# Optimization experiments

Hardware: AMD Instinct MI355X
Metric: run time of the kernel (lower is better)

Reference implementation:

```python
import jax, jax.numpy as jnp
import numpy as np

N_EMBD = 1024
N_HEAD = 16
HEAD_DIM = N_EMBD // N_HEAD


def setup_inputs() -> dict:
    key = jax.random.key(0)
    kx, kqkv, kw, kb = jax.random.split(key, 4)
    B, T = 4, 2048
    x = jax.random.normal(kx, (B, T, N_EMBD), dtype=jnp.float32)
    # nn.Linear weights stored [out, in]; apply as x @ W.T
    w_qkv = jax.random.normal(kqkv, (3 * N_EMBD, N_EMBD), dtype=jnp.float32) * (N_EMBD ** -0.5)
    w_out = jax.random.normal(kw, (N_EMBD, N_EMBD), dtype=jnp.float32) * (N_EMBD ** -0.5)
    b_out = jax.random.normal(kb, (N_EMBD,), dtype=jnp.float32) * 0.01
    return {"x": x, "w_qkv": w_qkv, "w_out": w_out, "b_out": b_out}


def reference(x, w_qkv, w_out, b_out):
    B, T, C = x.shape
    H, D = N_HEAD, HEAD_DIM
    qkv = jnp.einsum('btc,fc->btf', x, w_qkv)  # [B,T,3C]
    q, k, v = jnp.split(qkv, 3, axis=-1)
    q = q.reshape(B, T, H, D).transpose(0, 2, 1, 3)  # [B,H,T,D]
    k = k.reshape(B, T, H, D).transpose(0, 2, 1, 3)
    v = v.reshape(B, T, H, D).transpose(0, 2, 1, 3)
    att = jnp.einsum('bhqd,bhkd->bhqk', q, k) * (D ** -0.5)  # [B,H,T,T]
    causal = jnp.tril(jnp.ones((T, T), dtype=bool))
    att = jnp.where(causal[None, None], att, jnp.float32(-jnp.inf))
    att = jax.nn.softmax(att, axis=-1)
    out = jnp.einsum('bhqk,bhkd->bhqd', att, v)  # [B,H,T,D]
    out = out.transpose(0, 2, 1, 3).reshape(B, T, C)
    return jnp.einsum('btc,oc->bto', out, w_out) + b_out
```

## Files before the change

### kernel.cpp

```cpp
#include <hip/hip_runtime.h>
#include <stdint.h>

#define SEQ 2048
#define C3 3072
#define C1 1024

typedef __bf16 bf16x8 __attribute__((ext_vector_type(8)));
typedef short short8 __attribute__((ext_vector_type(8)));
typedef float f32x4 __attribute__((ext_vector_type(4)));
typedef float f32x16 __attribute__((ext_vector_type(16)));
typedef const __attribute__((address_space(1))) void gv_t;
typedef __attribute__((address_space(3))) void lv_t;

#if __has_builtin(__builtin_amdgcn_exp2f)
#define EXP2(x) __builtin_amdgcn_exp2f(x)
#else
#define EXP2(x) exp2f(x)
#endif

static __device__ __forceinline__ unsigned short f2bf(float f) {
  union { float ff; unsigned u; } x; x.ff = f;
  unsigned u = x.u + 0x7FFFu + ((x.u >> 16) & 1u);
  return (unsigned short)(u >> 16);
}
static __device__ __forceinline__ unsigned rne2(float lo, float hi) {
  return (unsigned)f2bf(lo) | ((unsigned)f2bf(hi) << 16);
}
static __device__ __forceinline__ unsigned pk2(float lo, float hi) {
  union { float f; unsigned u; } a, b; a.f = lo; b.f = hi;
  return __builtin_amdgcn_perm(b.u, a.u, 0x07060302);
}

__global__ void k_cvt3(const float* __restrict__ ia, const float* __restrict__ ib,
                       const float* __restrict__ ic, unsigned short* __restrict__ oa,
                       unsigned short* __restrict__ ob, unsigned short* __restrict__ oc) {
  int blk = blockIdx.x;
  const float* in; unsigned short* out; int base;
  if (blk < 8192)      { in = ia; out = oa; base = blk; }
  else if (blk < 11264){ in = ib; out = ob; base = blk - 8192; }
  else                 { in = ic; out = oc; base = blk - 11264; }
  int i = base * 256 + threadIdx.x;
  f32x4 v = ((const f32x4*)in)[i];
  ushort4 o;
  o.x = f2bf(v[0]); o.y = f2bf(v[1]); o.z = f2bf(v[2]); o.w = f2bf(v[3]);
  ((ushort4*)out)[i] = o;
}

template<int MODE>
__global__ __launch_bounds__(256, 3) void k_gemm(
    const unsigned short* __restrict__ A, const unsigned short* __restrict__ B,
    void* __restrict__ Cout, const float* __restrict__ bias,
    unsigned short* __restrict__ vTout, int M, int N, int K)
{
  __shared__ unsigned short As[128 * 64];
  __shared__ unsigned short Bs[128 * 64];
  const int tid = threadIdx.x;
  const int w = tid >> 6, l = tid & 63;
  const int lane15 = l & 15, quad = l >> 4;
  const int m0 = blockIdx.y * 128, n0 = blockIdx.x * 128;
  const int wm = (w >> 1) * 64, wn = (w & 1) * 64;

  f32x4 acc[4][4];
#pragma unroll
  for (int i = 0; i < 4; i++)
#pragma unroll
    for (int j = 0; j < 4; j++) acc[i][j] = (f32x4){0.f, 0.f, 0.f, 0.f};

  const int srow = l >> 3;
  const int g_off = ((l & 7) ^ (srow & 7)) * 8;
  const unsigned short* Ab = A + (size_t)(m0 + w * 32 + srow) * K + g_off;
  const unsigned short* Bb = B + (size_t)(n0 + w * 32 + srow) * K + g_off;
  const int rsl = lane15 & 7;

  for (int k0 = 0; k0 < K; k0 += 64) {
    __syncthreads();
#pragma unroll
    for (int i = 0; i < 4; i++) {
      int rb = w * 32 + i * 8;
      __builtin_amdgcn_global_load_lds((gv_t*)(Ab + (size_t)(i * 8) * K + k0),
                                       (lv_t*)&As[rb * 64], 16, 0, 0);
      __builtin_amdgcn_global_load_lds((gv_t*)(Bb + (size_t)(i * 8) * K + k0),
                                       (lv_t*)&Bs[rb * 64], 16, 0, 0);
    }
    __syncthreads();
#pragma unroll
    for (int s = 0; s < 2; s++) {
      bf16x8 af[4], bfr[4];
      const int slot = ((s * 4 + quad) ^ rsl) * 8;
#pragma unroll
      for (int t = 0; t < 4; t++) {
        af[t]  = *(const bf16x8*)&As[(wm + t * 16 + lane15) * 64 + slot];
        bfr[t] = *(const bf16x8*)&Bs[(wn + t * 16 + lane15) * 64 + slot];
      }
#pragma unroll
      for (int i = 0; i < 4; i++)
#pragma unroll
        for (int j = 0; j < 4; j++)
          acc[i][j] = __builtin_amdgcn_mfma_f32_16x16x32_bf16(af[i], bfr[j], acc[i][j], 0, 0, 0);
    }
  }

  if (MODE == 0) {
    if (n0 >= 2048) {
#pragma unroll
      for (int i = 0; i < 4; i++) {
        int rowb = m0 + wm + i * 16 + quad * 4;
        int bb = rowb >> 11, t = rowb & 2047;
#pragma unroll
        for (int j = 0; j < 4; j++) {
          int hd = n0 + wn + j * 16 + lane15 - 2048;
          unsigned short* vp = vTout +
              ((size_t)((bb << 4) + (hd >> 6)) * 64 + (hd & 63)) * SEQ + t;
          *(uint2*)vp = make_uint2(rne2(acc[i][j][0], acc[i][j][1]),
                                   rne2(acc[i][j][2], acc[i][j][3]));
        }
      }
    } else {
      unsigned short* Cp = (unsigned short*)Cout;
      const float s = (n0 < 1024) ? 0.18033688f : 1.0f;
#pragma unroll
      for (int i = 0; i < 4; i++) {
        int rowb = m0 + wm + i * 16 + quad * 4;
#pragma unroll
        for (int j = 0; j < 4; j++) {
          int col = n0 + wn + j * 16 + lane15;
#pragma unroll
          for (int r = 0; r < 4; r++)
            Cp[(size_t)(rowb + r) * N + col] = f2bf(acc[i][j][r] * s);
        }
      }
    }
  } else {
    float* Cp = (float*)Cout;
#pragma unroll
    for (int i = 0; i < 4; i++) {
      int rowb = m0 + wm + i * 16 + quad * 4;
#pragma unroll
      for (int j = 0; j < 4; j++) {
        int col = n0 + wn + j * 16 + lane15;
        float bv = bias[col];
#pragma unroll
        for (int r = 0; r < 4; r++)
          Cp[(size_t)(rowb + r) * N + col] = acc[i][j][r] + bv;
      }
    }
  }
}

__global__ __launch_bounds__(256, 4) void k_attn(
    const unsigned short* __restrict__ qkv, const unsigned short* __restrict__ vT,
    unsigned short* __restrict__ att)
{
  __shared__ unsigned short buf[16384];
  const int tid = threadIdx.x;
  const int w = tid >> 6, l = tid & 63;
  const int l31 = l & 31, hl = l >> 5;
  const int bh = blockIdx.x, b = bh >> 4, h = bh & 15;
  const int qt = (int)(gridDim.y - 1 - blockIdx.y);
  const int q0 = qt << 7;
  const int nkt = qt + 1;
  const size_t tokb = (size_t)b * SEQ;
  const int qmy = q0 + w * 32 + l31;

  bf16x8 qf[4];
  {
    const unsigned short* qp = qkv + (tokb + q0 + w * 32 + l31) * C3 + h * 64 + hl * 8;
#pragma unroll
    for (int ks = 0; ks < 4; ks++) qf[ks] = *(const bf16x8*)(qp + ks * 16);
  }

  f32x16 O[2];
#pragma unroll
  for (int i = 0; i < 16; i++) { O[0][i] = 0.f; O[1][i] = 0.f; }
  float lrun = 0.f;

  const int krow_l = l >> 3, kslot = l & 7;
  const int vrow_l = l >> 4, vslot = l & 15;
  unsigned short* Kb = &buf[0];
  unsigned short* Vb = &buf[8192];

  for (int kt = 0; kt < nkt; kt++) {
    const int k0 = kt << 7;
    __syncthreads();
#pragma unroll
    for (int i = 0; i < 4; i++) {
      int rb = (w * 4 + i) * 8;
      int row = rb + krow_l;
      int ck = kslot ^ (row & 7);
      const unsigned short* g = qkv + (tokb + k0 + row) * C3 + C1 + h * 64 + ck * 8;
      __builtin_amdgcn_global_load_lds((gv_t*)g, (lv_t*)&Kb[rb * 64], 16, 0, 0);
    }
#pragma unroll
    for (int i = 0; i < 4; i++) {
      int rb = (w * 4 + i) * 4;
      int row = rb + vrow_l;
      int ck = vslot ^ (row & 15);
      const unsigned short* g = vT + ((size_t)bh * 64 + row) * SEQ + k0 + ck * 8;
      __builtin_amdgcn_global_load_lds((gv_t*)g, (lv_t*)&Vb[rb * 128], 16, 0, 0);
    }
    __syncthreads();

    const bool diag = (kt == nkt - 1);

#pragma unroll
    for (int ht = 0; ht < 2; ht++) {
      if (diag && (ht * 2 > w)) continue;
      const bool two = !diag || (ht * 2 + 1 <= w);

#pragma unroll
      for (int lm = 0; lm < 2; lm++) {
        if (lm == 1 && !two) continue;
        const int mt = ht * 2 + lm;

        f32x16 stL;
#pragma unroll
        for (int i = 0; i < 16; i++) stL[i] = 0.f;
        {
          int row = mt * 32 + l31;
          const unsigned short* kr = &Kb[row * 64];
#pragma unroll
          for (int ks = 0; ks < 4; ks++) {
            bf16x8 a = *(const bf16x8*)&kr[((((ks << 1) | hl)) ^ (row & 7)) * 8];
            stL = __builtin_amdgcn_mfma_f32_32x32x16_bf16(a, qf[ks], stL, 0, 0, 0);
          }
        }

        if (diag && mt == w) {
#pragma unroll
          for (int r = 0; r < 16; r++) {
            int key = k0 + w * 32 + (r & 3) + ((r >> 2) << 3) + (hl << 2);
            if (key > qmy) stL[r] = -1e30f;
          }
        }

        float ps0 = 0.f, ps1 = 0.f, ps2 = 0.f, ps3 = 0.f;
        unsigned pk[8];
#pragma unroll
        for (int r = 0; r < 16; r += 4) {
          float p0 = EXP2(stL[r]     - 16.f);
          float p1 = EXP2(stL[r + 1] - 16.f);
          float p2 = EXP2(stL[r + 2] - 16.f);
          float p3 = EXP2(stL[r + 3] - 16.f);
          ps0 += p0; ps1 += p1; ps2 += p2; ps3 += p3;
          pk[(r >> 1)]     = pk2(p0, p1);
          pk[(r >> 1) + 1] = pk2(p2, p3);
        }
        lrun += (ps0 + ps1) + (ps2 + ps3);

#pragma unroll
        for (int e = 0; e < 2; e++) {
          unsigned pA0 = pk[4 * e], pA1 = pk[4 * e + 1];
          unsigned pB0 = pk[4 * e + 2], pB1 = pk[4 * e + 3];
          unsigned w0 = hl ? pA0 : pB0, w1 = hl ? pA1 : pB1;
          unsigned r0 = (unsigned)__shfl_xor((int)w0, 32, 64);
          unsigned r1 = (unsigned)__shfl_xor((int)w1, 32, 64);
          unsigned s0 = hl ? pB0 : pA0, s1 = hl ? pB1 : pA1;
          union { unsigned u[4]; bf16x8 v; } Bf;
          Bf.u[0] = hl ? r0 : s0; Bf.u[1] = hl ? r1 : s1;
          Bf.u[2] = hl ? s0 : r0; Bf.u[3] = hl ? s1 : r1;
          int kk = ht * 4 + lm * 2 + e;
#pragma unroll
          for (int dt = 0; dt < 2; dt++) {
            int row = dt * 32 + l31;
            bf16x8 a = *(const bf16x8*)&Vb[row * 128 + (((2 * kk + hl)) ^ (row & 15)) * 8];
            O[dt] = __builtin_amdgcn_mfma_f32_32x32x16_bf16(a, Bf.v, O[dt], 0, 0, 0);
          }
        }
      }
    }
  }

  lrun += __shfl_xor(lrun, 32, 64);

  __syncthreads();
  float linv = __builtin_amdgcn_rcpf(lrun);
  unsigned* epi32 = (unsigned*)&buf[0];
  const int base = w * 2304 + l31 * 72;
#pragma unroll
  for (int dt = 0; dt < 2; dt++)
#pragma unroll
    for (int c = 0; c < 4; c++) {
      int d0 = dt * 32 + c * 8 + hl * 4;
      epi32[(base + d0) >> 1]     = rne2(O[dt][4 * c] * linv, O[dt][4 * c + 1] * linv);
      epi32[(base + d0 + 2) >> 1] = rne2(O[dt][4 * c + 2] * linv, O[dt][4 * c + 3] * linv);
    }
  __builtin_amdgcn_s_waitcnt(0);
  {
    int q = l >> 1, hf = l & 1;
    const unsigned short* ep = &buf[w * 2304 + q * 72 + hf * 32];
    unsigned short* og = att + (tokb + q0 + w * 32 + q) * C1 + h * 64 + hf * 32;
#pragma unroll
    for (int c2 = 0; c2 < 4; c2++)
      *(bf16x8*)(og + c2 * 8) = *(const bf16x8*)&ep[c2 * 8];
  }
}

extern "C" void kernel_launch(void* const* d_in, const int* in_sizes, int n_in,
                              void* d_out, int out_size, void* d_ws, size_t ws_size,
                              hipStream_t stream) {
  const float* x     = (const float*)d_in[0];
  const float* w_qkv = (const float*)d_in[1];
  const float* w_out = (const float*)d_in[2];
  const float* b_out = (const float*)d_in[3];
  float* out = (float*)d_out;

  unsigned short* xb  = (unsigned short*)d_ws;
  unsigned short* wqb = xb  + (size_t)8192 * 1024;
  unsigned short* wob = wqb + (size_t)3072 * 1024;
  unsigned short* qkv = wob + (size_t)1024 * 1024;
  unsigned short* att = qkv + (size_t)8192 * 3072;
  unsigned short* vT  = att + (size_t)8192 * 1024;

  k_cvt3<<<12288, 256, 0, stream>>>(x, w_qkv, w_out, xb, wqb, wob);
  k_gemm<0><<<dim3(24, 64), 256, 0, stream>>>(xb, wqb, (void*)qkv, nullptr, vT, 8192, 3072, 1024);
  k_attn<<<dim3(64, 16), 256, 0, stream>>>(qkv, vT, att);
  k_gemm<1><<<dim3(8, 64), 256, 0, stream>>>(att, wob, (void*)out, b_out, nullptr, 8192, 1024, 1024);
}
```

Baseline: 230.3 us.

## Pair causal query tiles per block and double-buffer K/V staging

```diff
diff --git a/kernel.cpp b/kernel.cpp
--- a/kernel.cpp
+++ b/kernel.cpp
@@ -147,135 +147,119 @@
   }
 }
 
-__global__ __launch_bounds__(256, 4) void k_attn(
-    const unsigned short* __restrict__ qkv, const unsigned short* __restrict__ vT,
-    unsigned short* __restrict__ att)
-{
-  __shared__ unsigned short buf[16384];
-  const int tid = threadIdx.x;
-  const int w = tid >> 6, l = tid & 63;
-  const int l31 = l & 31, hl = l >> 5;
-  const int bh = blockIdx.x, b = bh >> 4, h = bh & 15;
-  const int qt = (int)(gridDim.y - 1 - blockIdx.y);
-  const int q0 = qt << 7;
-  const int nkt = qt + 1;
-  const size_t tokb = (size_t)b * SEQ;
-  const int qmy = q0 + w * 32 + l31;
-
-  bf16x8 qf[4];
-  {
-    const unsigned short* qp = qkv + (tokb + q0 + w * 32 + l31) * C3 + h * 64 + hl * 8;
-#pragma unroll
-    for (int ks = 0; ks < 4; ks++) qf[ks] = *(const bf16x8*)(qp + ks * 16);
-  }
-
-  f32x16 O[2];
-#pragma unroll
-  for (int i = 0; i < 16; i++) { O[0][i] = 0.f; O[1][i] = 0.f; }
-  float lrun = 0.f;
-
-  const int krow_l = l >> 3, kslot = l & 7;
-  const int vrow_l = l >> 4, vslot = l & 15;
-  unsigned short* Kb = &buf[0];
-  unsigned short* Vb = &buf[8192];
-
-  for (int kt = 0; kt < nkt; kt++) {
-    const int k0 = kt << 7;
-    __syncthreads();
-#pragma unroll
-    for (int i = 0; i < 4; i++) {
-      int rb = (w * 4 + i) * 8;
-      int row = rb + krow_l;
-      int ck = kslot ^ (row & 7);
-      const unsigned short* g = qkv + (tokb + k0 + row) * C3 + C1 + h * 64 + ck * 8;
-      __builtin_amdgcn_global_load_lds((gv_t*)g, (lv_t*)&Kb[rb * 64], 16, 0, 0);
-    }
-#pragma unroll
-    for (int i = 0; i < 4; i++) {
-      int rb = (w * 4 + i) * 4;
-      int row = rb + vrow_l;
-      int ck = vslot ^ (row & 15);
-      const unsigned short* g = vT + ((size_t)bh * 64 + row) * SEQ + k0 + ck * 8;
-      __builtin_amdgcn_global_load_lds((gv_t*)g, (lv_t*)&Vb[rb * 128], 16, 0, 0);
-    }
-    __syncthreads();
-
-    const bool diag = (kt == nkt - 1);
-
-#pragma unroll
-    for (int ht = 0; ht < 2; ht++) {
-      if (diag && (ht * 2 > w)) continue;
-      const bool two = !diag || (ht * 2 + 1 <= w);
-
-#pragma unroll
-      for (int lm = 0; lm < 2; lm++) {
-        if (lm == 1 && !two) continue;
-        const int mt = ht * 2 + lm;
-
-        f32x16 stL;
-#pragma unroll
-        for (int i = 0; i < 16; i++) stL[i] = 0.f;
-        {
-          int row = mt * 32 + l31;
-          const unsigned short* kr = &Kb[row * 64];
-#pragma unroll
-          for (int ks = 0; ks < 4; ks++) {
-            bf16x8 a = *(const bf16x8*)&kr[((((ks << 1) | hl)) ^ (row & 7)) * 8];
-            stL = __builtin_amdgcn_mfma_f32_32x32x16_bf16(a, qf[ks], stL, 0, 0, 0);
-          }
-        }
-
-        if (diag && mt == w) {
-#pragma unroll
-          for (int r = 0; r < 16; r++) {
-            int key = k0 + w * 32 + (r & 3) + ((r >> 2) << 3) + (hl << 2);
-            if (key > qmy) stL[r] = -1e30f;
-          }
-        }
-
-        float ps0 = 0.f, ps1 = 0.f, ps2 = 0.f, ps3 = 0.f;
-        unsigned pk[8];
-#pragma unroll
-        for (int r = 0; r < 16; r += 4) {
-          float p0 = EXP2(stL[r]     - 16.f);
-          float p1 = EXP2(stL[r + 1] - 16.f);
-          float p2 = EXP2(stL[r + 2] - 16.f);
-          float p3 = EXP2(stL[r + 3] - 16.f);
-          ps0 += p0; ps1 += p1; ps2 += p2; ps3 += p3;
-          pk[(r >> 1)]     = pk2(p0, p1);
-          pk[(r >> 1) + 1] = pk2(p2, p3);
-        }
-        lrun += (ps0 + ps1) + (ps2 + ps3);
-
-#pragma unroll
-        for (int e = 0; e < 2; e++) {
-          unsigned pA0 = pk[4 * e], pA1 = pk[4 * e + 1];
-          unsigned pB0 = pk[4 * e + 2], pB1 = pk[4 * e + 3];
-          unsigned w0 = hl ? pA0 : pB0, w1 = hl ? pA1 : pB1;
-          unsigned r0 = (unsigned)__shfl_xor((int)w0, 32, 64);
-          unsigned r1 = (unsigned)__shfl_xor((int)w1, 32, 64);
-          unsigned s0 = hl ? pB0 : pA0, s1 = hl ? pB1 : pA1;
-          union { unsigned u[4]; bf16x8 v; } Bf;
-          Bf.u[0] = hl ? r0 : s0; Bf.u[1] = hl ? r1 : s1;
-          Bf.u[2] = hl ? s0 : r0; Bf.u[3] = hl ? s1 : r1;
-          int kk = ht * 4 + lm * 2 + e;
-#pragma unroll
-          for (int dt = 0; dt < 2; dt++) {
-            int row = dt * 32 + l31;
-            bf16x8 a = *(const bf16x8*)&Vb[row * 128 + (((2 * kk + hl)) ^ (row & 15)) * 8];
-            O[dt] = __builtin_amdgcn_mfma_f32_32x32x16_bf16(a, Bf.v, O[dt], 0, 0, 0);
-          }
-        }
-      }
-    }
-  }
-
+
+static __device__ __forceinline__ void stage_kv(
+    unsigned short* bufp, const unsigned short* __restrict__ qkv,
+    const unsigned short* __restrict__ vT, size_t tokb, int bh, int h,
+    int k0, int w, int krow_l, int kslot, int vrow_l, int vslot)
+{
+  unsigned short* Kb = bufp;
+  unsigned short* Vb = bufp + 8192;
+#pragma unroll
+  for (int i = 0; i < 4; i++) {
+    int rb = (w * 4 + i) * 8;
+    int row = rb + krow_l;
+    int ck = kslot ^ (row & 7);
+    const unsigned short* g = qkv + (tokb + k0 + row) * C3 + C1 + h * 64 + ck * 8;
+    __builtin_amdgcn_global_load_lds((gv_t*)g, (lv_t*)&Kb[rb * 64], 16, 0, 0);
+  }
+#pragma unroll
+  for (int i = 0; i < 4; i++) {
+    int rb = (w * 4 + i) * 4;
+    int row = rb + vrow_l;
+    int ck = vslot ^ (row & 15);
+    const unsigned short* g = vT + ((size_t)bh * 64 + row) * SEQ + k0 + ck * 8;
+    __builtin_amdgcn_global_load_lds((gv_t*)g, (lv_t*)&Vb[rb * 128], 16, 0, 0);
+  }
+}
+
+static __device__ __forceinline__ void attn_tile(
+    f32x16* O, float& lrun, const bf16x8* qf,
+    const unsigned short* Kb, const unsigned short* Vb,
+    bool diag, int k0, int qmy, int w, int l31, int hl)
+{
+#pragma unroll
+  for (int ht = 0; ht < 2; ht++) {
+    if (diag && (ht * 2 > w)) continue;
+    const bool two = !diag || (ht * 2 + 1 <= w);
+
+#pragma unroll
+    for (int lm = 0; lm < 2; lm++) {
+      if (lm == 1 && !two) continue;
+      const int mt = ht * 2 + lm;
+
+      f32x16 stL;
+#pragma unroll
+      for (int i = 0; i < 16; i++) stL[i] = 0.f;
+      {
+        int row = mt * 32 + l31;
+        const unsigned short* kr = &Kb[row * 64];
+        __builtin_amdgcn_s_setprio(1);
+#pragma unroll
+        for (int ks = 0; ks < 4; ks++) {
+          bf16x8 a = *(const bf16x8*)&kr[((((ks << 1) | hl)) ^ (row & 7)) * 8];
+          stL = __builtin_amdgcn_mfma_f32_32x32x16_bf16(a, qf[ks], stL, 0, 0, 0);
+        }
+        __builtin_amdgcn_s_setprio(0);
+      }
+
+      if (diag && mt == w) {
+#pragma unroll
+        for (int r = 0; r < 16; r++) {
+          int key = k0 + w * 32 + (r & 3) + ((r >> 2) << 3) + (hl << 2);
+          if (key > qmy) stL[r] = -1e30f;
+        }
+      }
+
+      float ps0 = 0.f, ps1 = 0.f, ps2 = 0.f, ps3 = 0.f;
+      unsigned pk[8];
+#pragma unroll
+      for (int r = 0; r < 16; r += 4) {
+        float p0 = EXP2(stL[r]     - 16.f);
+        float p1 = EXP2(stL[r + 1] - 16.f);
+        float p2 = EXP2(stL[r + 2] - 16.f);
+        float p3 = EXP2(stL[r + 3] - 16.f);
+        ps0 += p0; ps1 += p1; ps2 += p2; ps3 += p3;
+        pk[(r >> 1)]     = pk2(p0, p1);
+        pk[(r >> 1) + 1] = pk2(p2, p3);
+      }
+      lrun += (ps0 + ps1) + (ps2 + ps3);
+
+#pragma unroll
+      for (int e = 0; e < 2; e++) {
+        unsigned pA0 = pk[4 * e], pA1 = pk[4 * e + 1];
+        unsigned pB0 = pk[4 * e + 2], pB1 = pk[4 * e + 3];
+        unsigned w0 = hl ? pA0 : pB0, w1 = hl ? pA1 : pB1;
+        unsigned r0 = (unsigned)__shfl_xor((int)w0, 32, 64);
+        unsigned r1 = (unsigned)__shfl_xor((int)w1, 32, 64);
+        unsigned s0 = hl ? pB0 : pA0, s1 = hl ? pB1 : pA1;
+        union { unsigned u[4]; bf16x8 v; } Bf;
+        Bf.u[0] = hl ? r0 : s0; Bf.u[1] = hl ? r1 : s1;
+        Bf.u[2] = hl ? s0 : r0; Bf.u[3] = hl ? s1 : r1;
+        int kk = ht * 4 + lm * 2 + e;
+        __builtin_amdgcn_s_setprio(1);
+#pragma unroll
+        for (int dt = 0; dt < 2; dt++) {
+          int row = dt * 32 + l31;
+          bf16x8 a = *(const bf16x8*)&Vb[row * 128 + (((2 * kk + hl)) ^ (row & 15)) * 8];
+          O[dt] = __builtin_amdgcn_mfma_f32_32x32x16_bf16(a, Bf.v, O[dt], 0, 0, 0);
+        }
+        __builtin_amdgcn_s_setprio(0);
+      }
+    }
+  }
+}
+
+static __device__ __forceinline__ void attn_epi(
+    const f32x16* O, float lrun, unsigned short* buf,
+    unsigned short* __restrict__ att, size_t tokb, int q0, int h,
+    int w, int l, int l31, int hl)
+{
   lrun += __shfl_xor(lrun, 32, 64);
-
-  __syncthreads();
   float linv = __builtin_amdgcn_rcpf(lrun);
-  unsigned* epi32 = (unsigned*)&buf[0];
+  unsigned* epi32 = (unsigned*)buf;
   const int base = w * 2304 + l31 * 72;
+  __builtin_amdgcn_s_waitcnt(0);
 #pragma unroll
   for (int dt = 0; dt < 2; dt++)
 #pragma unroll
@@ -293,6 +277,68 @@
     for (int c2 = 0; c2 < 4; c2++)
       *(bf16x8*)(og + c2 * 8) = *(const bf16x8*)&ep[c2 * 8];
   }
+}
+
+__global__ __launch_bounds__(256, 2) void k_attn(
+    const unsigned short* __restrict__ qkv, const unsigned short* __restrict__ vT,
+    unsigned short* __restrict__ att)
+{
+  __shared__ unsigned short buf[2][16384];
+  const int tid = threadIdx.x;
+  const int w = tid >> 6, l = tid & 63;
+  const int l31 = l & 31, hl = l >> 5;
+  const int bh = blockIdx.x, b = bh >> 4, h = bh & 15;
+  const int yq = blockIdx.y;
+  const int qt_lo = yq, qt_hi = 15 - yq;
+  const int q0l = qt_lo << 7, q0h = qt_hi << 7;
+  const int nkt = qt_hi + 1;
+  const size_t tokb = (size_t)b * SEQ;
+  const int qmy_l = q0l + w * 32 + l31;
+  const int qmy_h = q0h + w * 32 + l31;
+
+  const int krow_l = l >> 3, kslot = l & 7;
+  const int vrow_l = l >> 4, vslot = l & 15;
+
+  bf16x8 qfh[4], qfl[4];
+  {
+    const unsigned short* qph = qkv + (tokb + q0h + w * 32 + l31) * C3 + h * 64 + hl * 8;
+    const unsigned short* qpl = qkv + (tokb + q0l + w * 32 + l31) * C3 + h * 64 + hl * 8;
+#pragma unroll
+    for (int ks = 0; ks < 4; ks++) {
+      qfh[ks] = *(const bf16x8*)(qph + ks * 16);
+      qfl[ks] = *(const bf16x8*)(qpl + ks * 16);
+    }
+  }
+
+  f32x16 Oh[2], Ol[2];
+#pragma unroll
+  for (int i = 0; i < 16; i++) { Oh[0][i] = 0.f; Oh[1][i] = 0.f; Ol[0][i] = 0.f; Ol[1][i] = 0.f; }
+  float lrh = 0.f, lrl = 0.f;
+
+  stage_kv(&buf[0][0], qkv, vT, tokb, bh, h, 0, w, krow_l, kslot, vrow_l, vslot);
+
+  int cur = 0;
+  for (int kt = 0; kt < nkt; kt++) {
+    asm volatile("s_waitcnt vmcnt(0)" ::: "memory");
+    __builtin_amdgcn_s_barrier();
+    if (kt + 1 < nkt)
+      stage_kv(&buf[cur ^ 1][0], qkv, vT, tokb, bh, h, (kt + 1) << 7,
+               w, krow_l, kslot, vrow_l, vslot);
+
+    const unsigned short* Kb = &buf[cur][0];
+    const unsigned short* Vb = &buf[cur][8192];
+    const int k0 = kt << 7;
+
+    attn_tile(Oh, lrh, qfh, Kb, Vb, kt == qt_hi, k0, qmy_h, w, l31, hl);
+    if (kt <= qt_lo)
+      attn_tile(Ol, lrl, qfl, Kb, Vb, kt == qt_lo, k0, qmy_l, w, l31, hl);
+
+    cur ^= 1;
+  }
+
+  __syncthreads();
+  attn_epi(Oh, lrh, &buf[0][0], att, tokb, q0h, h, w, l, l31, hl);
+  attn_epi(Ol, lrl, &buf[0][0], att, tokb, q0l, h, w, l, l31, hl);
 }
 
 extern "C" void kernel_launch(void* const* d_in, const int* in_sizes, int n_in,
@@ -313,6 +359,6 @@
 
   k_cvt3<<<12288, 256, 0, stream>>>(x, w_qkv, w_out, xb, wqb, wob);
   k_gemm<0><<<dim3(24, 64), 256, 0, stream>>>(xb, wqb, (void*)qkv, nullptr, vT, 8192, 3072, 1024);
-  k_attn<<<dim3(64, 16), 256, 0, stream>>>(qkv, vT, att);
+  k_attn<<<dim3(64, 8), 256, 0, stream>>>(qkv, vT, att);
   k_gemm<1><<<dim3(8, 64), 256, 0, stream>>>(att, wob, (void*)out, b_out, nullptr, 8192, 1024, 1024);
 }
```

New measurement: 234.5 us. About the same (+1.8%).
